# Kernel optimization log

Hardware: AMD Instinct MI355X
Metric: run time of the kernel (lower is better)

The kernel has to match this reference:

```python
import jax, jax.numpy as jnp
import numpy as np

CLASSES = 256
SUPERCLASSES = 16
CLASS_FACTOR = CLASSES // SUPERCLASSES
HEIGHT = 448
WIDTH = 160
BATCH = 1
CH_IN = 128
CH_R0 = 256
CH_R1 = 8


def _leaky(v):
    return jnp.where(v >= 0, v, 0.01 * v)


def _grouped1x1(x, W, b):
    # x: (B, H, Cin, W_sp); W: (H, Cout, Cin); b: (H, Cout)
    return jnp.einsum('bhcw,hoc->bhow', x, W) + b[None, :, :, None]


def setup_inputs() -> dict:
    key = jax.random.key(0)
    ks = jax.random.split(key, 16)
    s = 0.05
    return {
        'x_in': jax.random.normal(ks[0], (BATCH, CH_IN, HEIGHT, WIDTH), jnp.float32),
        'W_cl1': jax.random.normal(ks[1], (HEIGHT, 128, CH_IN), jnp.float32) * s,
        'b_cl1': jax.random.normal(ks[2], (HEIGHT, 128), jnp.float32) * s,
        'W_cl2': jax.random.normal(ks[3], (HEIGHT, 128, 128), jnp.float32) * s,
        'b_cl2': jax.random.normal(ks[4], (HEIGHT, 128), jnp.float32) * s,
        'W_cl3': jax.random.normal(ks[5], (HEIGHT, 128, 128), jnp.float32) * s,
        'b_cl3': jax.random.normal(ks[6], (HEIGHT, 128), jnp.float32) * s,
        'W_cl4': jax.random.normal(ks[7], (HEIGHT, CLASSES + 1, 128), jnp.float32) * s,
        'b_cl4': jax.random.normal(ks[8], (HEIGHT, CLASSES + 1), jnp.float32) * s,
        'W_reg1': jax.random.normal(ks[9], (HEIGHT, CH_R0, CH_IN), jnp.float32) * s,
        'b_reg1': jax.random.normal(ks[10], (HEIGHT, CH_R0), jnp.float32) * s,
        'W_cm2': jax.random.normal(ks[11], (SUPERCLASSES * HEIGHT, CH_R0, CH_R1), jnp.float32) * s,
        'b_cm2': jax.random.normal(ks[12], (SUPERCLASSES * HEIGHT, CH_R1), jnp.float32) * s,
        'W_cm3': jax.random.normal(ks[13], (CLASSES * HEIGHT, CH_R1, 1), jnp.float32) * s,
        'b_cm3': jax.random.normal(ks[14], (CLASSES * HEIGHT, 1), jnp.float32) * s,
    }


def reference(x_in, W_cl1, b_cl1, W_cl2, b_cl2, W_cl3, b_cl3, W_cl4, b_cl4,
              W_reg1, b_reg1, W_cm2, b_cm2, W_cm3, b_cm3):
    B, C, H, Wd = x_in.shape
    x = x_in.transpose(0, 2, 1, 3)  # (B, H, C, W) == grouped-conv layout
    x_r = _leaky(_grouped1x1(x, W_reg1, b_reg1))  # (B, H, CH_R0, W)
    # classification branch
    h = _leaky(_grouped1x1(x, W_cl1, b_cl1))
    h = _leaky(_grouped1x1(h, W_cl2, b_cl2))
    h = _leaky(_grouped1x1(h, W_cl3, b_cl3))
    h = _grouped1x1(h, W_cl4, b_cl4)  # (B, H, CLASSES+1, W)
    logits = h.transpose(0, 2, 1, 3)  # (B, CLASSES+1, H, W)
    cls = logits[:, :CLASSES]
    mask = _leaky(logits[:, -1:])  # (B, 1, H, W)
    inds = jnp.argmax(cls, axis=1)[:, None]  # (B, 1, H, W)
    offs = jnp.arange(H)[None, None, :, None]
    # NOTE: original flattens indices in (b, h, w) order...
    inds_r = (inds + offs * CLASSES).reshape(-1).astype(jnp.int32)
    inds_sc = (inds // CLASS_FACTOR + offs * SUPERCLASSES).reshape(-1).astype(jnp.int32)
    # ...while CondMul input rows come in (b, w, h) order (faithful to torch code).
    xr_rows = x_r.transpose(0, 3, 1, 2).reshape(-1, CH_R0)  # (B*W*H, CH_R0)
    y = _leaky(jnp.einsum('nc,nco->no', xr_rows, W_cm2[inds_sc]) + b_cm2[inds_sc])
    r = jnp.einsum('nc,nco->no', y, W_cm3[inds_r]) + b_cm3[inds_r]  # (N, 1)
    r = r.reshape(B, Wd, H, 1).transpose(0, 3, 2, 1)  # (B, 1, H, W)
    x_real = (inds.astype(jnp.float32) + r) * (1.0 / CLASSES)
    return x_real, mask
```

## Files before the change

### kernel.cpp

```cpp
#include <hip/hip_runtime.h>
#include <hip/hip_bf16.h>

#define HH 448
#define WW 160
#define NPIX (HH*WW)

typedef unsigned long long u64;
typedef _Float16 h8 __attribute__((ext_vector_type(8)));
typedef _Float16 h4 __attribute__((ext_vector_type(4)));
typedef float f32x4 __attribute__((ext_vector_type(4)));

#define MFMA16(A,B,C) __builtin_amdgcn_mfma_f32_16x16x32_f16(A,B,C,0,0,0)
#define LO_SCALE 4096.0f
#define LO_INV   (1.0f/4096.0f)

__device__ __forceinline__ float leaky(float v) { return v >= 0.f ? v : 0.01f * v; }

__device__ __forceinline__ u64 packKey(float m, int r) {
    unsigned u = __float_as_uint(m);
    u = (u & 0x80000000u) ? ~u : (u | 0x80000000u);
    return ((u64)u << 32) | (unsigned)(255 - r);
}

__device__ __forceinline__ _Float16 splitHi(float v) { return (_Float16)v; }
__device__ __forceinline__ _Float16 splitLo(float v, _Float16 hi) {
    return (_Float16)((v - (float)hi) * LO_SCALE);
}

__device__ __forceinline__ void cvtA(const float4& v0, const float4& v1, h8& ah, h8& al) {
    const float v[8] = {v0.x,v0.y,v0.z,v0.w,v1.x,v1.y,v1.z,v1.w};
#pragma unroll
    for (int j = 0; j < 8; ++j) {
        const _Float16 hi = splitHi(v[j]);
        ah[j] = hi;
        al[j] = splitLo(v[j], hi);
    }
}

__device__ __forceinline__ void gemmPass(const _Float16* lah, const _Float16* lal,
                                         const float* __restrict__ Wp,
                                         int lrow, int lg, int col0,
                                         f32x4 aH[2][5], f32x4 aL[2][5])
{
    const f32x4 zero = {0.f, 0.f, 0.f, 0.f};
#pragma unroll
    for (int i = 0; i < 2; ++i)
#pragma unroll
        for (int c = 0; c < 5; ++c) { aH[i][c] = zero; aL[i][c] = zero; }

    const float* wb0 = Wp + lrow * 128 + lg * 8;
    const float* wb1 = Wp + (16 + lrow) * 128 + lg * 8;
    float4 n00 = *(const float4*)(wb0);
    float4 n01 = *(const float4*)(wb0 + 4);
    float4 n10 = *(const float4*)(wb1);
    float4 n11 = *(const float4*)(wb1 + 4);

#pragma unroll 1
    for (int s = 0; s < 4; ++s) {
        const float4 c00 = n00, c01 = n01, c10 = n10, c11 = n11;
        if (s < 3) {
            n00 = *(const float4*)(wb0 + (s + 1) * 32);
            n01 = *(const float4*)(wb0 + (s + 1) * 32 + 4);
            n10 = *(const float4*)(wb1 + (s + 1) * 32);
            n11 = *(const float4*)(wb1 + (s + 1) * 32 + 4);
        }
        h8 Ah[2], Al[2];
        cvtA(c00, c01, Ah[0], Al[0]);
        cvtA(c10, c11, Ah[1], Al[1]);

        h8 Bh[5], Bl[5];
        const int gg = (s << 2) + lg;
#pragma unroll
        for (int c = 0; c < 5; ++c) {
            const int u = gg * 160 + col0 + (c << 4) + lrow;
            Bh[c] = *(const h8*)(lah + (u << 3));
            Bl[c] = *(const h8*)(lal + (u << 3));
        }
#pragma unroll
        for (int i = 0; i < 2; ++i)
#pragma unroll
            for (int c = 0; c < 5; ++c) {
                aH[i][c] = MFMA16(Ah[i], Bh[c], aH[i][c]);
                aL[i][c] = MFMA16(Ah[i], Bl[c], aL[i][c]);
                aL[i][c] = MFMA16(Al[i], Bh[c], aL[i][c]);
            }
    }
}

__global__ __launch_bounds__(512, 2) void kA(
    const float* __restrict__ x_in,
    const float* __restrict__ Wcl1, const float* __restrict__ bcl1,
    const float* __restrict__ Wcl2, const float* __restrict__ bcl2,
    const float* __restrict__ Wcl3, const float* __restrict__ bcl3,
    const float* __restrict__ Wcl4, const float* __restrict__ bcl4,
    const float* __restrict__ Wreg1, const float* __restrict__ breg1,
    __hip_bfloat16* __restrict__ xr, int* __restrict__ ind, float* __restrict__ out)
{
    __shared__ _Float16 lah[16 * 160 * 8];
    __shared__ _Float16 lal[16 * 160 * 8];
    __shared__ u64 argb[160];

    const int h = blockIdx.x;
    const int t = threadIdx.x;
    const int wvid = t >> 6;
    const int l = t & 63;
    const int lrow = l & 15, lg = l >> 4;
    const int rtp = wvid >> 1;
    const int ch = wvid & 1;
    const int col0 = ch * 80;
    const int trb = rtp * 32;

    if (t < 160) argb[t] = 0ull;

#pragma unroll 1
    for (int k = 0; k < 5; ++k) {
        const int id = t + (k << 9);
        const int g = id / 160, col = id - g * 160;
        float v[8];
#pragma unroll
        for (int j = 0; j < 8; ++j)
            v[j] = x_in[(size_t)(g * 8 + j) * 71680 + h * 160 + col];
        h8 hh, ll;
#pragma unroll
        for (int j = 0; j < 8; ++j) {
            const _Float16 hi = splitHi(v[j]);
            hh[j] = hi;
            ll[j] = splitLo(v[j], hi);
        }
        const int u = g * 160 + col;
        *(h8*)(lah + (u << 3)) = hh;
        *(h8*)(lal + (u << 3)) = ll;
    }
    __syncthreads();

    {
        const float* W1 = Wreg1 + (size_t)h * 32768;
        const float* b1 = breg1 + h * 256;
#pragma unroll 1
        for (int p = 0; p < 2; ++p) {
            const int rowOff = (p << 7) + trb;
            f32x4 aH[2][5], aL[2][5];
            gemmPass(lah, lal, W1 + rowOff * 128, lrow, lg, col0, aH, aL);
#pragma unroll
            for (int i = 0; i < 2; ++i) {
                const int r0 = rowOff + (i << 4) + (lg << 2);
                const float4 bb = *(const float4*)&b1[r0];
#pragma unroll
                for (int c = 0; c < 5; ++c) {
                    const int col = col0 + (c << 4) + lrow;
                    alignas(8) unsigned short us[4];
#pragma unroll
                    for (int r = 0; r < 4; ++r) {
                        const float a = aH[i][c][r] + aL[i][c][r] * LO_INV + ((const float*)&bb)[r];
                        __hip_bfloat16 bv = __float2bfloat16(leaky(a));
                        us[r] = *(const unsigned short*)&bv;
                    }
                    *(uint2*)(xr + (((size_t)(h * 160 + col)) << 8) + r0) = *(const uint2*)us;
                }
            }
        }
    }

#pragma unroll 1
    for (int L = 0; L < 3; ++L) {
        const float* W = (L == 0) ? Wcl1 + (size_t)h * 16384
                       : (L == 1) ? Wcl2 + (size_t)h * 16384
                                  : Wcl3 + (size_t)h * 16384;
        const float* b = (L == 0) ? bcl1 + (h << 7)
                       : (L == 1) ? bcl2 + (h << 7)
                                  : bcl3 + (h << 7);
        f32x4 aH[2][5], aL[2][5];
        gemmPass(lah, lal, W + trb * 128, lrow, lg, col0, aH, aL);
        float nv[2][5][4];
#pragma unroll
        for (int i = 0; i < 2; ++i) {
            const int r0 = trb + (i << 4) + (lg << 2);
            const float4 bb = *(const float4*)&b[r0];
#pragma unroll
            for (int c = 0; c < 5; ++c)
#pragma unroll
                for (int r = 0; r < 4; ++r)
                    nv[i][c][r] = leaky(aH[i][c][r] + aL[i][c][r] * LO_INV + ((const float*)&bb)[r]);
        }
        __syncthreads();
#pragma unroll
        for (int i = 0; i < 2; ++i) {
            const int r0 = trb + (i << 4) + (lg << 2);
            const int g = r0 >> 3, off = r0 & 7;
#pragma unroll
            for (int c = 0; c < 5; ++c) {
                const int col = col0 + (c << 4) + lrow;
                h4 wh, wl;
#pragma unroll
                for (int r = 0; r < 4; ++r) {
                    const _Float16 hi = splitHi(nv[i][c][r]);
                    wh[r] = hi;
                    wl[r] = splitLo(nv[i][c][r], hi);
                }
                *(h4*)(lah + ((g * 160 + col) << 3) + off) = wh;
                *(h4*)(lal + ((g * 160 + col) << 3) + off) = wl;
            }
        }
        __syncthreads();
    }

    {
        const float* W4 = Wcl4 + (size_t)h * 32896;
        const float* b4 = bcl4 + h * 257;
        float mv[5]; int mr[5];
#pragma unroll
        for (int c = 0; c < 5; ++c) { mv[c] = -3.4e38f; mr[c] = 0; }
#pragma unroll 1
        for (int p = 0; p < 2; ++p) {
            const int rowOff = (p << 7) + trb;
            f32x4 aH[2][5], aL[2][5];
            gemmPass(lah, lal, W4 + rowOff * 128, lrow, lg, col0, aH, aL);
#pragma unroll
            for (int i = 0; i < 2; ++i) {
                const int r0 = rowOff + (i << 4) + (lg << 2);
                const float4 bb = *(const float4*)&b4[r0];
#pragma unroll
                for (int c = 0; c < 5; ++c)
#pragma unroll
                    for (int r = 0; r < 4; ++r) {
                        const float a = aH[i][c][r] + aL[i][c][r] * LO_INV + ((const float*)&bb)[r];
                        if (a > mv[c]) { mv[c] = a; mr[c] = r0 + r; }
                    }
            }
        }
#pragma unroll
        for (int c = 0; c < 5; ++c)
            atomicMax(&argb[col0 + (c << 4) + lrow], packKey(mv[c], mr[c]));
    }
    __syncthreads();

    if (t < 160) {
        const u64 kk = argb[t];
        ind[h * 160 + t] = 255 - (int)(kk & 0xFFu);
        const float* Wm = Wcl4 + (size_t)h * 32896 + 32768;
        float accm = 0.f;
#pragma unroll 2
        for (int g = 0; g < 16; ++g) {
            const h8 hv = *(const h8*)(lah + ((g * 160 + t) << 3));
            const h8 lv = *(const h8*)(lal + ((g * 160 + t) << 3));
            const float4 w0 = *(const float4*)&Wm[g * 8];
            const float4 w1 = *(const float4*)&Wm[g * 8 + 4];
            const float wv[8] = {w0.x,w0.y,w0.z,w0.w,w1.x,w1.y,w1.z,w1.w};
#pragma unroll
            for (int j = 0; j < 8; ++j)
                accm = fmaf(wv[j], (float)hv[j] + (float)lv[j] * LO_INV, accm);
        }
        out[NPIX + h * 160 + t] = leaky(accm + bcl4[h * 257 + 256]);
    }
}

__global__ __launch_bounds__(256) void kB(
    const __hip_bfloat16* __restrict__ xr, const int* __restrict__ ind,
    const float* __restrict__ Wcm2, const float* __restrict__ bcm2,
    const float* __restrict__ Wcm3, const float* __restrict__ bcm3,
    float* __restrict__ out)
{
    const int gwave = (int)((blockIdx.x * blockDim.x + threadIdx.x) >> 6);
    const int lane = threadIdx.x & 63;
    const int nwave = (int)(gridDim.x * (blockDim.x >> 6));

    for (int n = gwave; n < NPIX; n += nwave) {
        const int h_o = n % HH, w_o = n / HH;
        const int h_i = n / WW, w_i = n % WW;
        const int ig = ind[h_i * WW + w_i];
        const int sc = (ig >> 4) + (h_i << 4);
        const int rr = ig + (h_i << 8);

        const __hip_bfloat16* xp = xr + (size_t)(h_o * WW + w_o) * 256;
        const float* Wp = Wcm2 + (size_t)sc * 2048;

        float acc[8];
#pragma unroll
        for (int o = 0; o < 8; ++o) acc[o] = 0.f;

        const int c0 = lane * 4;
        const ushort4 xv4 = *(const ushort4*)((const unsigned short*)xp + c0);
        float xf[4];
        xf[0] = __uint_as_float((unsigned int)xv4.x << 16);
        xf[1] = __uint_as_float((unsigned int)xv4.y << 16);
        xf[2] = __uint_as_float((unsigned int)xv4.z << 16);
        xf[3] = __uint_as_float((unsigned int)xv4.w << 16);

#pragma unroll
        for (int i = 0; i < 4; ++i) {
            const float4* wrow = (const float4*)&Wp[(c0 + i) * 8];
            const float4 wa = wrow[0];
            const float4 wb_ = wrow[1];
            const float x = xf[i];
            acc[0] += x * wa.x;  acc[1] += x * wa.y;  acc[2] += x * wa.z;  acc[3] += x * wa.w;
            acc[4] += x * wb_.x; acc[5] += x * wb_.y; acc[6] += x * wb_.z; acc[7] += x * wb_.w;
        }
#pragma unroll
        for (int o = 0; o < 8; ++o) {
            float v = acc[o];
#pragma unroll
            for (int d = 32; d > 0; d >>= 1) v += __shfl_xor(v, d, 64);
            acc[o] = v;
        }
        float r = bcm3[rr];
        const float* b2 = bcm2 + (size_t)sc * 8;
        const float* w3 = Wcm3 + (size_t)rr * 8;
#pragma unroll
        for (int o = 0; o < 8; ++o) {
            const float y = leaky(acc[o] + b2[o]);
            r += y * w3[o];
        }
        if (lane == 0) {
            const float iv = (float)ind[h_o * WW + w_o];
            out[h_o * WW + w_o] = (iv + r) * (1.0f / 256.0f);
        }
    }
}

extern "C" void kernel_launch(void* const* d_in, const int* in_sizes, int n_in,
                              void* d_out, int out_size, void* d_ws, size_t ws_size,
                              hipStream_t stream)
{
    const float* x_in  = (const float*)d_in[0];
    const float* Wcl1  = (const float*)d_in[1];
    const float* bcl1  = (const float*)d_in[2];
    const float* Wcl2  = (const float*)d_in[3];
    const float* bcl2  = (const float*)d_in[4];
    const float* Wcl3  = (const float*)d_in[5];
    const float* bcl3  = (const float*)d_in[6];
    const float* Wcl4  = (const float*)d_in[7];
    const float* bcl4  = (const float*)d_in[8];
    const float* Wreg1 = (const float*)d_in[9];
    const float* breg1 = (const float*)d_in[10];
    const float* Wcm2  = (const float*)d_in[11];
    const float* bcm2  = (const float*)d_in[12];
    const float* Wcm3  = (const float*)d_in[13];
    const float* bcm3  = (const float*)d_in[14];

    float* out = (float*)d_out;

    __hip_bfloat16* xr = (__hip_bfloat16*)d_ws;
    int* ind = (int*)((char*)d_ws + (size_t)NPIX * 256 * sizeof(__hip_bfloat16));

    kA<<<dim3(HH), dim3(512), 0, stream>>>(x_in, Wcl1, bcl1, Wcl2, bcl2, Wcl3, bcl3,
                                           Wcl4, bcl4, Wreg1, breg1, xr, ind, out);
    kB<<<dim3(1792), dim3(256), 0, stream>>>(xr, ind, Wcm2, bcm2, Wcm3, bcm3, out);
}
```

Before: 188.3 us.

## Split each row across two 256-thread blocks covering half the width

Kernel A now launches two blocks per image row, each handling 80 columns with 4 waves instead of one 512-thread block handling all 160 columns. This halves shared memory per block and raises the grid to 896 blocks, so more blocks fit per CU and the 256 CUs get a better load balance than with 448 blocks. Block ids are interleaved so that both halves of a row run close together. The cost is that each row's weight matrices are fetched twice from global/L2, one by each half-block.

After: 202.3 us. +7.4%, slower.

```diff
diff --git a/kernel.cpp b/kernel.cpp
--- a/kernel.cpp
+++ b/kernel.cpp
@@ -4,6 +4,7 @@
 #define HH 448
 #define WW 160
 #define NPIX (HH*WW)
+#define BCOL 80
 
 typedef unsigned long long u64;
 typedef _Float16 h8 __attribute__((ext_vector_type(8)));
@@ -39,7 +40,7 @@
 
 __device__ __forceinline__ void gemmPass(const _Float16* lah, const _Float16* lal,
                                          const float* __restrict__ Wp,
-                                         int lrow, int lg, int col0,
+                                         int lrow, int lg,
                                          f32x4 aH[2][5], f32x4 aL[2][5])
 {
     const f32x4 zero = {0.f, 0.f, 0.f, 0.f};
@@ -72,7 +73,7 @@
         const int gg = (s << 2) + lg;
 #pragma unroll
         for (int c = 0; c < 5; ++c) {
-            const int u = gg * 160 + col0 + (c << 4) + lrow;
+            const int u = gg * BCOL + (c << 4) + lrow;
             Bh[c] = *(const h8*)(lah + (u << 3));
             Bl[c] = *(const h8*)(lal + (u << 3));
         }
@@ -87,7 +88,7 @@
     }
 }
 
-__global__ __launch_bounds__(512, 2) void kA(
+__global__ __launch_bounds__(256, 3) void kA(
     const float* __restrict__ x_in,
     const float* __restrict__ Wcl1, const float* __restrict__ bcl1,
     const float* __restrict__ Wcl2, const float* __restrict__ bcl2,
@@ -96,30 +97,30 @@
     const float* __restrict__ Wreg1, const float* __restrict__ breg1,
     __hip_bfloat16* __restrict__ xr, int* __restrict__ ind, float* __restrict__ out)
 {
-    __shared__ _Float16 lah[16 * 160 * 8];
-    __shared__ _Float16 lal[16 * 160 * 8];
-    __shared__ u64 argb[160];
-
-    const int h = blockIdx.x;
+    __shared__ _Float16 lah[16 * BCOL * 8];
+    __shared__ _Float16 lal[16 * BCOL * 8];
+    __shared__ u64 argb[BCOL];
+
+    const int bid = blockIdx.x;
+    const int h = ((bid >> 4) << 3) | (bid & 7);
+    const int w0 = ((bid >> 3) & 1) * BCOL;
+
     const int t = threadIdx.x;
     const int wvid = t >> 6;
     const int l = t & 63;
     const int lrow = l & 15, lg = l >> 4;
-    const int rtp = wvid >> 1;
-    const int ch = wvid & 1;
-    const int col0 = ch * 80;
-    const int trb = rtp * 32;
-
-    if (t < 160) argb[t] = 0ull;
+    const int trb = wvid * 32;
+
+    if (t < BCOL) argb[t] = 0ull;
 
 #pragma unroll 1
     for (int k = 0; k < 5; ++k) {
-        const int id = t + (k << 9);
-        const int g = id / 160, col = id - g * 160;
+        const int id = t + (k << 8);
+        const int g = id / BCOL, col = id - g * BCOL;
         float v[8];
 #pragma unroll
         for (int j = 0; j < 8; ++j)
-            v[j] = x_in[(size_t)(g * 8 + j) * 71680 + h * 160 + col];
+            v[j] = x_in[(size_t)(g * 8 + j) * 71680 + h * 160 + w0 + col];
         h8 hh, ll;
 #pragma unroll
         for (int j = 0; j < 8; ++j) {
@@ -127,7 +128,7 @@
             hh[j] = hi;
             ll[j] = splitLo(v[j], hi);
         }
-        const int u = g * 160 + col;
+        const int u = g * BCOL + col;
         *(h8*)(lah + (u << 3)) = hh;
         *(h8*)(lal + (u << 3)) = ll;
     }
@@ -140,14 +141,14 @@
         for (int p = 0; p < 2; ++p) {
             const int rowOff = (p << 7) + trb;
             f32x4 aH[2][5], aL[2][5];
-            gemmPass(lah, lal, W1 + rowOff * 128, lrow, lg, col0, aH, aL);
+            gemmPass(lah, lal, W1 + rowOff * 128, lrow, lg, aH, aL);
 #pragma unroll
             for (int i = 0; i < 2; ++i) {
                 const int r0 = rowOff + (i << 4) + (lg << 2);
                 const float4 bb = *(const float4*)&b1[r0];
 #pragma unroll
                 for (int c = 0; c < 5; ++c) {
-                    const int col = col0 + (c << 4) + lrow;
+                    const int col = w0 + (c << 4) + lrow;
                     alignas(8) unsigned short us[4];
 #pragma unroll
                     for (int r = 0; r < 4; ++r) {
@@ -170,7 +171,7 @@
                        : (L == 1) ? bcl2 + (h << 7)
                                   : bcl3 + (h << 7);
         f32x4 aH[2][5], aL[2][5];
-        gemmPass(lah, lal, W + trb * 128, lrow, lg, col0, aH, aL);
+        gemmPass(lah, lal, W + trb * 128, lrow, lg, aH, aL);
         float nv[2][5][4];
 #pragma unroll
         for (int i = 0; i < 2; ++i) {
@@ -189,7 +190,7 @@
             const int g = r0 >> 3, off = r0 & 7;
 #pragma unroll
             for (int c = 0; c < 5; ++c) {
-                const int col = col0 + (c << 4) + lrow;
+                const int col = (c << 4) + lrow;
                 h4 wh, wl;
 #pragma unroll
                 for (int r = 0; r < 4; ++r) {
@@ -197,8 +198,8 @@
                     wh[r] = hi;
                     wl[r] = splitLo(nv[i][c][r], hi);
                 }
-                *(h4*)(lah + ((g * 160 + col) << 3) + off) = wh;
-                *(h4*)(lal + ((g * 160 + col) << 3) + off) = wl;
+                *(h4*)(lah + ((g * BCOL + col) << 3) + off) = wh;
+                *(h4*)(lal + ((g * BCOL + col) << 3) + off) = wl;
             }
         }
         __syncthreads();
@@ -214,7 +215,7 @@
         for (int p = 0; p < 2; ++p) {
             const int rowOff = (p << 7) + trb;
             f32x4 aH[2][5], aL[2][5];
-            gemmPass(lah, lal, W4 + rowOff * 128, lrow, lg, col0, aH, aL);
+            gemmPass(lah, lal, W4 + rowOff * 128, lrow, lg, aH, aL);
 #pragma unroll
             for (int i = 0; i < 2; ++i) {
                 const int r0 = rowOff + (i << 4) + (lg << 2);
@@ -230,27 +231,27 @@
         }
 #pragma unroll
         for (int c = 0; c < 5; ++c)
-            atomicMax(&argb[col0 + (c << 4) + lrow], packKey(mv[c], mr[c]));
+            atomicMax(&argb[(c << 4) + lrow], packKey(mv[c], mr[c]));
     }
     __syncthreads();
 
-    if (t < 160) {
+    if (t < BCOL) {
         const u64 kk = argb[t];
-        ind[h * 160 + t] = 255 - (int)(kk & 0xFFu);
+        ind[h * 160 + w0 + t] = 255 - (int)(kk & 0xFFu);
         const float* Wm = Wcl4 + (size_t)h * 32896 + 32768;
         float accm = 0.f;
 #pragma unroll 2
         for (int g = 0; g < 16; ++g) {
-            const h8 hv = *(const h8*)(lah + ((g * 160 + t) << 3));
-            const h8 lv = *(const h8*)(lal + ((g * 160 + t) << 3));
-            const float4 w0 = *(const float4*)&Wm[g * 8];
-            const float4 w1 = *(const float4*)&Wm[g * 8 + 4];
-            const float wv[8] = {w0.x,w0.y,w0.z,w0.w,w1.x,w1.y,w1.z,w1.w};
+            const h8 hv = *(const h8*)(lah + ((g * BCOL + t) << 3));
+            const h8 lv = *(const h8*)(lal + ((g * BCOL + t) << 3));
+            const float4 w0v = *(const float4*)&Wm[g * 8];
+            const float4 w1v = *(const float4*)&Wm[g * 8 + 4];
+            const float wv[8] = {w0v.x,w0v.y,w0v.z,w0v.w,w1v.x,w1v.y,w1v.z,w1v.w};
 #pragma unroll
             for (int j = 0; j < 8; ++j)
                 accm = fmaf(wv[j], (float)hv[j] + (float)lv[j] * LO_INV, accm);
         }
-        out[NPIX + h * 160 + t] = leaky(accm + bcl4[h * 257 + 256]);
+        out[NPIX + h * 160 + w0 + t] = leaky(accm + bcl4[h * 257 + 256]);
     }
 }
 
@@ -342,7 +343,7 @@
     __hip_bfloat16* xr = (__hip_bfloat16*)d_ws;
     int* ind = (int*)((char*)d_ws + (size_t)NPIX * 256 * sizeof(__hip_bfloat16));
 
-    kA<<<dim3(HH), dim3(512), 0, stream>>>(x_in, Wcl1, bcl1, Wcl2, bcl2, Wcl3, bcl3,
-                                           Wcl4, bcl4, Wreg1, breg1, xr, ind, out);
+    kA<<<dim3(HH * 2), dim3(256), 0, stream>>>(x_in, Wcl1, bcl1, Wcl2, bcl2, Wcl3, bcl3,
+                                               Wcl4, bcl4, Wreg1, breg1, xr, ind, out);
     kB<<<dim3(1792), dim3(256), 0, stream>>>(xr, ind, Wcm2, bcm2, Wcm3, bcm3, out);
 }
```
